# Kernel tuning notes

Measured on AMD Instinct MI355X. Metric: run time of the kernel, lower is better.

## Reference

```python
import jax, jax.numpy as jnp
import numpy as np

B, N, H = 8, 512, 256
D2 = H // 2          # per-direction hidden = attention proj = 128
VOCAB, EMB = 100, 256
DIN0 = EMB + 3


def _sru_pp_layer(x, pad, Wq, Wk, Wv, Wu, vf, vr, bf, br):
    # x: (L, Bt, din); pad: (L, Bt) bool, True = padded position
    L, Bt, _ = x.shape
    d2 = Wu.shape[1] // 8
    q = x @ Wq                                   # (L,Bt,proj) attention projection
    k = q @ Wk
    v = q @ Wv
    scale = 1.0 / jnp.sqrt(jnp.asarray(q.shape[-1], q.dtype))
    scores = jnp.einsum('lbp,mbp->blm', q, k) * scale
    scores = jnp.where(pad.T[:, None, :], -1e9, scores)
    a = jnp.einsum('blm,mbp->lbp', jax.nn.softmax(scores, axis=-1), v) + q
    U = (a @ Wu).reshape(L, Bt, 2, 4, d2)        # 2 directions x 4 matrices

    def run_dir(Ud, padd, vf_d, vr_d, bf_d, br_d):
        def step(c, inp):
            u, p = inp                            # u: (Bt,4,d2), p: (Bt,)
            f = jax.nn.sigmoid(u[:, 1] + vf_d * c + bf_d)
            r = jax.nn.sigmoid(u[:, 2] + vr_d * c + br_d)
            c_new = f * c + (1.0 - f) * u[:, 0]
            c_new = jnp.where(p[:, None], c, c_new)
            h = jnp.where(p[:, None], 0.0, r * c_new + (1.0 - r) * u[:, 3])
            return c_new, h
        c0 = jnp.zeros((Bt, d2), x.dtype)
        _, hs = jax.lax.scan(step, c0, (Ud, padd))
        return hs

    hf = run_dir(U[:, :, 0], pad, vf[0], vr[0], bf[0], br[0])
    hb = run_dir(U[::-1, :, 1], pad[::-1], vf[1], vr[1], bf[1], br[1])[::-1]
    return jnp.concatenate([hf, hb], axis=-1)     # (L,Bt,2*d2)


def _forward(noisy_seqs, noisy_cords, mask, emb, params):
    Bb, Nn = noisy_seqs.shape
    X = noisy_cords[:, :, 1]                      # CA coordinates (B,N,3)
    m3 = mask[..., None]
    center = (X * m3).sum(1) / m3.sum(1)
    Xc = X - center[:, None] * m3
    C = jnp.einsum('bni,bnj->bij', Xc, Xc)        # (B,3,3) covariance
    _, V = jnp.linalg.eigh(jax.lax.stop_gradient(C))
    ops = jnp.asarray([[i, j, k] for i in (-1, 1) for j in (-1, 1) for k in (-1, 1)], X.dtype)
    F_ops = ops[None, :, None, :] * V[:, None]    # (B,8,3,3) sign-flipped frames
    hX = jnp.einsum('boji,bpj->bopi', F_ops, Xc).reshape(Bb * 8, Nn, 3)
    seq = jnp.where(noisy_seqs < 0, 82, noisy_seqs)
    hS = jnp.broadcast_to(emb[seq][:, None], (Bb, 8, Nn, emb.shape[1])).reshape(Bb * 8, Nn, -1)
    h = jnp.swapaxes(jnp.concatenate([hX, hS], -1), 0, 1)   # (N, B*8, EMB+3)
    pad = jnp.broadcast_to((mask == 0.0)[:, None], (Bb, 8, Nn)).reshape(Bb * 8, Nn).T
    for p in params:
        h = _sru_pp_layer(h, pad, *p)
    return jnp.swapaxes(h, 0, 1).reshape(Bb, 8, Nn, -1).mean(1)


def setup_inputs():
    key = jax.random.key(0)
    ks = [jax.random.fold_in(key, i) for i in range(32)]
    inp = {
        'noisy_seqs': jax.random.randint(ks[0], (B, N), 0, VOCAB, dtype=jnp.int32),
        'noisy_cords': jax.random.normal(ks[1], (B, N, 4, 3), jnp.float32),
        'mask': jnp.ones((B, N), jnp.float32),
        'emb': 0.02 * jax.random.normal(ks[2], (VOCAB, EMB), jnp.float32),
    }
    i = 3
    for l, din in enumerate([DIN0, H]):
        inp[f'Wq{l}'] = jax.random.normal(ks[i], (din, D2), jnp.float32) / np.sqrt(din); i += 1
        inp[f'Wk{l}'] = jax.random.normal(ks[i], (D2, D2), jnp.float32) / np.sqrt(D2); i += 1
        inp[f'Wv{l}'] = jax.random.normal(ks[i], (D2, D2), jnp.float32) / np.sqrt(D2); i += 1
        inp[f'Wu{l}'] = jax.random.normal(ks[i], (D2, 8 * D2), jnp.float32) / np.sqrt(D2); i += 1
        inp[f'vf{l}'] = 0.1 * jax.random.normal(ks[i], (2, D2), jnp.float32); i += 1
        inp[f'vr{l}'] = 0.1 * jax.random.normal(ks[i], (2, D2), jnp.float32); i += 1
        inp[f'bf{l}'] = jnp.zeros((2, D2), jnp.float32)
        inp[f'br{l}'] = jnp.zeros((2, D2), jnp.float32)
    return inp


def reference(noisy_seqs, noisy_cords, mask, emb,
              Wq0, Wk0, Wv0, Wu0, vf0, vr0, bf0, br0,
              Wq1, Wk1, Wv1, Wu1, vf1, vr1, bf1, br1):
    params = [(Wq0, Wk0, Wv0, Wu0, vf0, vr0, bf0, br0),
              (Wq1, Wk1, Wv1, Wu1, vf1, vr1, bf1, br1)]
    return _forward(noisy_seqs, noisy_cords, mask, emb, params)
```

## Files before the change

### kernel.cpp

```cpp
#include <hip/hip_runtime.h>
#include <hip/hip_bf16.h>
#include <math.h>

#define L_    512
#define F_    64
#define M_    (F_*L_)
#define D2_   128
#define H_    256
#define LOG2E_ 1.4426950408889634f

typedef unsigned short u16;
typedef __attribute__((ext_vector_type(8))) short s16x8;
typedef __attribute__((ext_vector_type(4))) float f32x4;

__device__ inline u16 bf_hi(float x) {
  union { float f; unsigned u; } v; v.f = x;
  unsigned r = v.u + 0x7fffu + ((v.u >> 16) & 1u);
  return (u16)(r >> 16);
}
__device__ inline float bf_to_f(u16 h) {
  union { float f; unsigned u; } v; v.u = ((unsigned)h) << 16; return v.f;
}
__device__ inline void split2(float x, u16& h, u16& l) {
  h = bf_hi(x);
  l = bf_hi(x - bf_to_f(h));
}
__device__ inline float exp2_fast(float x) {
#if __has_builtin(__builtin_amdgcn_exp2f)
  return __builtin_amdgcn_exp2f(x);
#else
  return __expf(x * 0.6931471805599453f);
#endif
}
__device__ inline float rcp_fast(float x) {
#if __has_builtin(__builtin_amdgcn_rcpf)
  return __builtin_amdgcn_rcpf(x);
#else
  return 1.f/x;
#endif
}

#define RSPLIT_A 18432
#define RSPLIT_B 26624

__global__ void geom_kernel(const float* __restrict__ cords, const float* __restrict__ mask,
                            float* __restrict__ misc) {
  int b = blockIdx.x;
  int t = threadIdx.x;
  __shared__ float red[4][256];
  float sx=0.f, sy=0.f, sz=0.f, sm=0.f;
  for (int l = t; l < 512; l += 256) {
    float m = mask[b*512 + l];
    const float* X = cords + ((size_t)(b*512 + l)*4 + 1)*3;
    sx += X[0]*m; sy += X[1]*m; sz += X[2]*m; sm += m;
  }
  red[0][t]=sx; red[1][t]=sy; red[2][t]=sz; red[3][t]=sm;
  __syncthreads();
  for (int off=128; off>0; off>>=1) {
    if (t < off) { red[0][t]+=red[0][t+off]; red[1][t]+=red[1][t+off];
                   red[2][t]+=red[2][t+off]; red[3][t]+=red[3][t+off]; }
    __syncthreads();
  }
  float inv = 1.f/red[3][0];
  float cx = red[0][0]*inv, cy = red[1][0]*inv, cz = red[2][0]*inv;
  __syncthreads();
  __shared__ float red6[6][256];
  float c00=0,c01=0,c02=0,c11=0,c12=0,c22=0;
  for (int l = t; l < 512; l += 256) {
    float m = mask[b*512+l];
    const float* X = cords + ((size_t)(b*512+l)*4 + 1)*3;
    float x = X[0]-cx*m, y = X[1]-cy*m, z = X[2]-cz*m;
    c00+=x*x; c01+=x*y; c02+=x*z; c11+=y*y; c12+=y*z; c22+=z*z;
  }
  red6[0][t]=c00; red6[1][t]=c01; red6[2][t]=c02;
  red6[3][t]=c11; red6[4][t]=c12; red6[5][t]=c22;
  __syncthreads();
  for (int off=128; off>0; off>>=1) {
    if (t < off) for (int j=0;j<6;j++) red6[j][t]+=red6[j][t+off];
    __syncthreads();
  }
  if (t == 0) {
    double A[3][3], V[3][3];
    A[0][0]=red6[0][0]; A[0][1]=A[1][0]=red6[1][0]; A[0][2]=A[2][0]=red6[2][0];
    A[1][1]=red6[3][0]; A[1][2]=A[2][1]=red6[4][0]; A[2][2]=red6[5][0];
    for (int j=0;j<3;j++) for (int i=0;i<3;i++) V[j][i] = (i==j)?1.0:0.0;
    for (int sweep=0; sweep<10; ++sweep) {
      for (int p=0;p<2;p++) for (int q=p+1;q<3;q++) {
        double apq = A[p][q];
        if (fabs(apq) < 1e-18) continue;
        double app = A[p][p], aqq = A[q][q];
        double tau = (aqq - app) / (2.0*apq);
        double tt = (tau >= 0.0) ? 1.0/(tau + sqrt(1.0+tau*tau))
                                 : 1.0/(tau - sqrt(1.0+tau*tau));
        double cc = 1.0/sqrt(1.0+tt*tt), ss = tt*cc;
        A[p][p] = app - tt*apq;
        A[q][q] = aqq + tt*apq;
        A[p][q] = A[q][p] = 0.0;
        int r = 3 - p - q;
        double arp = A[r][p], arq = A[r][q];
        A[r][p] = A[p][r] = cc*arp - ss*arq;
        A[r][q] = A[q][r] = ss*arp + cc*arq;
        for (int rr2=0; rr2<3; ++rr2) {
          double vrp = V[rr2][p], vrq = V[rr2][q];
          V[rr2][p] = cc*vrp - ss*vrq;
          V[rr2][q] = ss*vrp + cc*vrq;
        }
      }
    }
    double w[3] = {A[0][0], A[1][1], A[2][2]};
    int idx[3] = {0,1,2};
    for (int i=0;i<2;i++) for (int j=0;j<2-i;j++)
      if (w[idx[j]] > w[idx[j+1]]) { int tmp=idx[j]; idx[j]=idx[j+1]; idx[j+1]=tmp; }
    for (int jj=0;jj<3;jj++) for (int ii=0;ii<3;ii++)
      misc[b*12 + jj*3 + ii] = (float)V[jj][idx[ii]];
    misc[b*12+9]=cx; misc[b*12+10]=cy; misc[b*12+11]=cz;
  }
}

__global__ void build_h0(const int* __restrict__ seqs, const float* __restrict__ cords,
                         const float* __restrict__ mask, const float* __restrict__ emb,
                         const float* __restrict__ misc,
                         u16* __restrict__ h0h, u16* __restrict__ h0l) {
  int t = threadIdx.x;
  int r = blockIdx.x*4 + (t >> 6);
  int lane = t & 63;
  int f = r >> 9, l = r & 511;
  int b = f >> 3, o = f & 7;
  u16* rh = h0h + (size_t)r * 288;
  u16* rl = h0l + (size_t)r * 288;
  if (lane == 0) {
    float m = mask[b*512 + l];
    const float* X = cords + ((size_t)(b*512 + l)*4 + 1)*3;
    const float* mb = misc + b*12;
    float x = X[0]-mb[9]*m, y = X[1]-mb[10]*m, z = X[2]-mb[11]*m;
    #pragma unroll
    for (int i=0;i<3;i++) {
      float sgn = ((o >> (2-i)) & 1) ? 1.f : -1.f;
      float val = sgn * (mb[0+i]*x + mb[3+i]*y + mb[6+i]*z);
      u16 h,lo; split2(val,h,lo); rh[i]=h; rl[i]=lo;
    }
  }
  if (lane < 29) { rh[259+lane] = 0; rl[259+lane] = 0; }
  int s = seqs[b*512 + l];
  if (s < 0) s = 82;
  const float4 e4 = *((const float4*)(emb + (size_t)s*256) + lane);
  float ev[4] = {e4.x, e4.y, e4.z, e4.w};
  #pragma unroll
  for (int i=0;i<4;i++) {
    u16 h,lo; split2(ev[i],h,lo);
    rh[3 + lane*4 + i] = h; rl[3 + lane*4 + i] = lo;
  }
}

__global__ void prep_wqkv_mul(const float* __restrict__ Wq, const float* __restrict__ Wk,
                              const float* __restrict__ Wv,
                              float* __restrict__ wqk, float* __restrict__ wqv) {
  int k = blockIdx.x;
  int y = blockIdx.y;
  int t = threadIdx.x;
  __shared__ float row[128];
  row[t] = Wq[(size_t)k*128 + t];
  __syncthreads();
  const float* W2 = y ? Wv : Wk;
  float acc = 0.f;
  for (int j = 0; j < 128; j++) acc += row[j] * W2[(size_t)j*128 + t];
  (y ? wqv : wqk)[(size_t)k*128 + t] = acc;
}

__global__ void prep_wT3(const float* __restrict__ Wq, const float* __restrict__ wqk,
                         const float* __restrict__ wqv,
                         u16* __restrict__ Th, u16* __restrict__ Tl,
                         int K, int KP) {
  int y = blockIdx.y;
  int n = blockIdx.x;
  const float* W = (y==0) ? Wq : (y==1) ? wqk : wqv;
  int row = y*128 + n;
  for (int k = threadIdx.x; k < KP; k += 128) {
    float x = (k < K) ? W[(size_t)k*128 + n] : 0.f;
    u16 h,l; split2(x,h,l);
    Th[(size_t)row*KP + k] = h; Tl[(size_t)row*KP + k] = l;
  }
}

__global__ void prep_wu(const float* __restrict__ Wu, u16* __restrict__ Th, u16* __restrict__ Tl,
                        const float* __restrict__ bfv, const float* __restrict__ brv,
                        float* __restrict__ nbf, float* __restrict__ nbr) {
  int n = blockIdx.x;
  int dir = blockIdx.y;
  int k = threadIdx.x;
  int d = n >> 2, g = n & 3;
  float x = Wu[(size_t)k*1024 + (dir*4+g)*128 + d];
  if (g == 1 || g == 2) x *= -LOG2E_;
  u16 h,l; split2(x,h,l);
  size_t o = ((size_t)dir*512 + n)*128 + k;
  Th[o]=h; Tl[o]=l;
  if (n == 0) {
    nbf[dir*128 + k] = bfv[dir*128 + k] * (-LOG2E_);
    nbr[dir*128 + k] = brv[dir*128 + k] * (-LOG2E_);
  }
}

template<int EPI>
__global__ __launch_bounds__(256) void gemm_bb(
    const u16* __restrict__ Ah, const u16* __restrict__ Al,
    const u16* __restrict__ Bh, const u16* __restrict__ Bl,
    int KP, int lda, int ldb,
    long aBatch, long bBatch, long cBatch,
    u16* __restrict__ Ch, u16* __restrict__ Cl, int ldc,
    u16* __restrict__ Dh, u16* __restrict__ Dl,
    u16* __restrict__ Eh, u16* __restrict__ El,
    float* __restrict__ F0, float* __restrict__ F1, float* __restrict__ F2,
    float* __restrict__ F3, float* __restrict__ F4, float* __restrict__ F5,
    const u16* __restrict__ rh, const u16* __restrict__ rl,
    const float* __restrict__ maskp, const float* __restrict__ nbf,
    const float* __restrict__ nbr, float scale, int dirOff)
{
  __shared__ u16 As[2][128][40];
  __shared__ u16 Bs[2][128][40];
  __shared__ float epsM[128];
  __shared__ float epsA[128];
  const int t = threadIdx.x;
  const int z = blockIdx.z;
  const int bm = blockIdx.x * 128, bn = blockIdx.y * 128;
  Ah += (size_t)z * aBatch; Al += (size_t)z * aBatch;
  Bh += (size_t)z * bBatch; Bl += (size_t)z * bBatch;

  const int lane = t & 63;
  const int w = t >> 6, wr = w >> 1, wc = w & 1;
  const int fr = lane & 15, g = lane >> 4;

  const bool isD1 = (bn >= 512);
  const int dirU = dirOff + (isD1 ? 1 : 0);
  if (EPI == 4) {
    if (t < 128) {
      int r = bm + t;
      epsM[t] = maskp[(r >> 12)*512 + (r & 511)];
      int nl = (bn + t) & 511;
      int dd = nl >> 2, gg2 = nl & 3;
      epsA[t] = (gg2==1) ? nbf[dirU*128 + dd] : (gg2==2) ? nbr[dirU*128 + dd] : 0.f;
    }
  }

  f32x4 acc[4][4] = {};

  for (int k0 = 0; k0 < KP; k0 += 32) {
    #pragma unroll
    for (int cc = 0; cc < 2; cc++) {
      int c = t + cc*256;
      int m = c >> 2, sub = c & 3;
      const size_t ga = (size_t)(bm + m)*lda + k0 + sub*8;
      const size_t gb = (size_t)(bn + m)*ldb + k0 + sub*8;
      *(int4*)&As[0][m][sub*8] = *(const int4*)(Ah + ga);
      *(int4*)&As[1][m][sub*8] = *(const int4*)(Al + ga);
      *(int4*)&Bs[0][m][sub*8] = *(const int4*)(Bh + gb);
      *(int4*)&Bs[1][m][sub*8] = *(const int4*)(Bl + gb);
    }
    __syncthreads();
    s16x8 af[4][2], bfr[4][2];
    #pragma unroll
    for (int i = 0; i < 4; i++) {
      af[i][0]  = *(const s16x8*)&As[0][wr*64 + i*16 + fr][g*8];
      af[i][1]  = *(const s16x8*)&As[1][wr*64 + i*16 + fr][g*8];
      bfr[i][0] = *(const s16x8*)&Bs[0][wc*64 + i*16 + fr][g*8];
      bfr[i][1] = *(const s16x8*)&Bs[1][wc*64 + i*16 + fr][g*8];
    }
    #pragma unroll
    for (int mi = 0; mi < 4; mi++)
      #pragma unroll
      for (int nj = 0; nj < 4; nj++)
        acc[mi][nj] = __builtin_amdgcn_mfma_f32_16x16x32_bf16(af[mi][0], bfr[nj][0], acc[mi][nj], 0,0,0);
    #pragma unroll
    for (int mi = 0; mi < 4; mi++)
      #pragma unroll
      for (int nj = 0; nj < 4; nj++)
        acc[mi][nj] = __builtin_amdgcn_mfma_f32_16x16x32_bf16(af[mi][0], bfr[nj][1], acc[mi][nj], 0,0,0);
    #pragma unroll
    for (int mi = 0; mi < 4; mi++)
      #pragma unroll
      for (int nj = 0; nj < 4; nj++)
        acc[mi][nj] = __builtin_amdgcn_mfma_f32_16x16x32_bf16(af[mi][1], bfr[nj][0], acc[mi][nj], 0,0,0);
    __syncthreads();
  }

  const int rbase = bm + wr*64, nbase = bn + wc*64;
  float* tA = isD1 ? F3 : F0;
  float* tB = isD1 ? F4 : F1;
  float* tC = isD1 ? F5 : F2;
  const int gg = fr & 3;
  const float ovr = (gg==1) ? -16384.f : (gg==2) ? 16384.f : 0.f;

  #pragma unroll
  for (int mi = 0; mi < 4; mi++) {
    #pragma unroll
    for (int nj = 0; nj < 4; nj++) {
      #pragma unroll
      for (int rg = 0; rg < 4; rg++) {
        int r = rbase + mi*16 + g*4 + rg;
        int n = nbase + nj*16 + fr;
        float val = acc[mi][nj][rg];
        if (EPI == 2) {
          float vv = val * scale;
          if (maskp[(z>>3)*512 + n] == 0.f) vv = -1e9f;
          F0[(size_t)z*cBatch + (size_t)r*ldc + n] = vv;
        } else if (EPI == 3) {
          size_t o = (size_t)z*cBatch + (size_t)r*ldc + n;
          float vv = val + (bf_to_f(rh[o]) + bf_to_f(rl[o]));
          u16 h,l; split2(vv,h,l);
          Ch[o]=h; Cl[o]=l;
        } else if (EPI == 4) {
          int nloc = (n & 511);
          val += epsA[n - bn];
          if (epsM[r - bm] == 0.f) val = ovr;
          float* Up;
          if (r < RSPLIT_A)      Up = tA + (size_t)r*512;
          else if (r < RSPLIT_B) Up = tB + (size_t)(r - RSPLIT_A)*512;
          else                   Up = tC + (size_t)(r - RSPLIT_B)*512;
          Up[nloc] = val;
        } else {
          u16 h,l; split2(val,h,l);
          if (blockIdx.y == 0) {
            size_t o = (size_t)r*128 + n;
            Ch[o]=h; Cl[o]=l;
          } else if (blockIdx.y == 1) {
            size_t o = (size_t)r*128 + (n - 128);
            Dh[o]=h; Dl[o]=l;
          } else {
            size_t o = ((size_t)(r >> 9)*128 + (n - 256))*512 + (r & 511);
            Eh[o]=h; El[o]=l;
          }
        }
      }
    }
  }
}

__global__ __launch_bounds__(256) void attn_flash(
    const u16* __restrict__ qh, const u16* __restrict__ ql,
    const u16* __restrict__ kh, const u16* __restrict__ kl,
    const u16* __restrict__ vTh, const u16* __restrict__ vTl,
    const float* __restrict__ maskp,
    u16* __restrict__ ah, u16* __restrict__ al, float scale)
{
  __shared__ u16 As[2][64][36];
  __shared__ u16 Bs[2][128][36];
  __shared__ u16 Ps[2][64][68];
  __shared__ float rmaxL[2][64];
  __shared__ float rsumL[2][64];
  __shared__ float mskt[64];
  const int t = threadIdx.x;
  const int bid = blockIdx.x;
  const int xcd  = bid & 7;
  const int rest = bid >> 3;
  const int tile = rest & 7;
  const int f    = (rest >> 3)*8 + xcd;
  const int bq = f >> 3;
  const int bm = tile * 64;
  const size_t qrow0 = (size_t)f*512 + bm;
  const int lane = t & 63;
  const int w = t >> 6, wr = w >> 1, wc = w & 1;
  const int fr = lane & 15, g = lane >> 4;
  const int m_ = t >> 2, sub_ = t & 3;

  float mrun[2][4], srun[2][4];
  #pragma unroll
  for (int mi=0;mi<2;mi++)
    #pragma unroll
    for (int rg=0;rg<4;rg++) { mrun[mi][rg] = -3e38f; srun[mi][rg] = 0.f; }
  f32x4 Oacc[2][4] = {};

  for (int kt = 0; kt < 8; ++kt) {
    if (t < 64) mskt[t] = maskp[bq*512 + kt*64 + t];
    f32x4 Sacc[2][2] = {};
    #pragma unroll
    for (int k0 = 0; k0 < 4; ++k0) {
      {
        const size_t ga = (qrow0 + m_)*128 + k0*32 + sub_*8;
        const size_t gb = ((size_t)f*512 + kt*64 + m_)*128 + k0*32 + sub_*8;
        *(int4*)&As[0][m_][sub_*8] = *(const int4*)(qh + ga);
        *(int4*)&As[1][m_][sub_*8] = *(const int4*)(ql + ga);
        *(int4*)&Bs[0][m_][sub_*8] = *(const int4*)(kh + gb);
        *(int4*)&Bs[1][m_][sub_*8] = *(const int4*)(kl + gb);
      }
      __syncthreads();
      s16x8 af[2][2], bf2[2][2];
      #pragma unroll
      for (int i = 0; i < 2; i++) {
        af[i][0]  = *(const s16x8*)&As[0][wr*32 + i*16 + fr][g*8];
        af[i][1]  = *(const s16x8*)&As[1][wr*32 + i*16 + fr][g*8];
        bf2[i][0] = *(const s16x8*)&Bs[0][wc*32 + i*16 + fr][g*8];
        bf2[i][1] = *(const s16x8*)&Bs[1][wc*32 + i*16 + fr][g*8];
      }
      #pragma unroll
      for (int mi = 0; mi < 2; mi++)
        #pragma unroll
        for (int nj = 0; nj < 2; nj++)
          Sacc[mi][nj] = __builtin_amdgcn_mfma_f32_16x16x32_bf16(af[mi][0], bf2[nj][0], Sacc[mi][nj], 0,0,0);
      #pragma unroll
      for (int mi = 0; mi < 2; mi++)
        #pragma unroll
        for (int nj = 0; nj < 2; nj++)
          Sacc[mi][nj] = __builtin_amdgcn_mfma_f32_16x16x32_bf16(af[mi][0], bf2[nj][1], Sacc[mi][nj], 0,0,0);
      #pragma unroll
      for (int mi = 0; mi < 2; mi++)
        #pragma unroll
        for (int nj = 0; nj < 2; nj++)
          Sacc[mi][nj] = __builtin_amdgcn_mfma_f32_16x16x32_bf16(af[mi][1], bf2[nj][0], Sacc[mi][nj], 0,0,0);
      __syncthreads();
    }
    float mkv[2];
    mkv[0] = mskt[wc*32 + fr];
    mkv[1] = mskt[wc*32 + 16 + fr];
    float rm[2][4];
    #pragma unroll
    for (int mi=0;mi<2;mi++)
      #pragma unroll
      for (int rg=0;rg<4;rg++) rm[mi][rg] = -3e38f;
    #pragma unroll
    for (int mi=0;mi<2;mi++)
      #pragma unroll
      for (int nj=0;nj<2;nj++)
        #pragma unroll
        for (int rg=0;rg<4;rg++) {
          float sv = Sacc[mi][nj][rg]*scale;
          sv = (mkv[nj]==0.f) ? -1e9f : sv;
          Sacc[mi][nj][rg] = sv;
          rm[mi][rg] = fmaxf(rm[mi][rg], sv);
        }
    #pragma unroll
    for (int off=1; off<16; off<<=1)
      #pragma unroll
      for (int mi=0;mi<2;mi++)
        #pragma unroll
        for (int rg=0;rg<4;rg++) rm[mi][rg] = fmaxf(rm[mi][rg], __shfl_xor(rm[mi][rg], off));
    if (fr == 0) {
      #pragma unroll
      for (int mi=0;mi<2;mi++)
        #pragma unroll
        for (int rg=0;rg<4;rg++) rmaxL[wc][wr*32 + mi*16 + g*4 + rg] = rm[mi][rg];
    }
    __syncthreads();
    float alpha[2][4], rs[2][4];
    #pragma unroll
    for (int mi=0;mi<2;mi++)
      #pragma unroll
      for (int rg=0;rg<4;rg++) {
        int rl_ = wr*32 + mi*16 + g*4 + rg;
        float tmax = fmaxf(rmaxL[0][rl_], rmaxL[1][rl_]);
        float mn = fmaxf(mrun[mi][rg], tmax);
        alpha[mi][rg] = exp2_fast((mrun[mi][rg] - mn)*LOG2E_);
        mrun[mi][rg] = mn;
        rs[mi][rg] = 0.f;
      }
    #pragma unroll
    for (int mi=0;mi<2;mi++)
      #pragma unroll
      for (int nj=0;nj<2;nj++)
        #pragma unroll
        for (int rg=0;rg<4;rg++) {
          float p = exp2_fast((Sacc[mi][nj][rg] - mrun[mi][rg])*LOG2E_);
          rs[mi][rg] += p;
          u16 h,l; split2(p,h,l);
          int rl_ = wr*32 + mi*16 + g*4 + rg;
          int cl_ = wc*32 + nj*16 + fr;
          Ps[0][rl_][cl_] = h;
          Ps[1][rl_][cl_] = l;
        }
    #pragma unroll
    for (int off=1; off<16; off<<=1)
      #pragma unroll
      for (int mi=0;mi<2;mi++)
        #pragma unroll
        for (int rg=0;rg<4;rg++) rs[mi][rg] += __shfl_xor(rs[mi][rg], off);
    if (fr == 0) {
      #pragma unroll
      for (int mi=0;mi<2;mi++)
        #pragma unroll
        for (int rg=0;rg<4;rg++) rsumL[wc][wr*32 + mi*16 + g*4 + rg] = rs[mi][rg];
    }
    #pragma unroll
    for (int mi=0;mi<2;mi++)
      #pragma unroll
      for (int nj=0;nj<4;nj++)
        #pragma unroll
        for (int rg=0;rg<4;rg++) Oacc[mi][nj][rg] *= alpha[mi][rg];
    __syncthreads();
    #pragma unroll
    for (int mi=0;mi<2;mi++)
      #pragma unroll
      for (int rg=0;rg<4;rg++) {
        int rl_ = wr*32 + mi*16 + g*4 + rg;
        srun[mi][rg] = srun[mi][rg]*alpha[mi][rg] + rsumL[0][rl_] + rsumL[1][rl_];
      }
    #pragma unroll
    for (int k0 = 0; k0 < 2; ++k0) {
      #pragma unroll
      for (int cc = 0; cc < 2; cc++) {
        int c = t + cc*256;
        int mv = c >> 2, sb = c & 3;
        const size_t gv = ((size_t)f*128 + mv)*512 + kt*64 + k0*32 + sb*8;
        *(int4*)&Bs[0][mv][sb*8] = *(const int4*)(vTh + gv);
        *(int4*)&Bs[1][mv][sb*8] = *(const int4*)(vTl + gv);
      }
      __syncthreads();
      s16x8 pa[2][2], pb[4][2];
      #pragma unroll
      for (int i = 0; i < 2; i++) {
        pa[i][0] = *(const s16x8*)&Ps[0][wr*32 + i*16 + fr][k0*32 + g*8];
        pa[i][1] = *(const s16x8*)&Ps[1][wr*32 + i*16 + fr][k0*32 + g*8];
      }
      #pragma unroll
      for (int j = 0; j < 4; j++) {
        pb[j][0] = *(const s16x8*)&Bs[0][wc*64 + j*16 + fr][g*8];
        pb[j][1] = *(const s16x8*)&Bs[1][wc*64 + j*16 + fr][g*8];
      }
      #pragma unroll
      for (int mi = 0; mi < 2; mi++)
        #pragma unroll
        for (int nj = 0; nj < 4; nj++)
          Oacc[mi][nj] = __builtin_amdgcn_mfma_f32_16x16x32_bf16(pa[mi][0], pb[nj][0], Oacc[mi][nj], 0,0,0);
      #pragma unroll
      for (int mi = 0; mi < 2; mi++)
        #pragma unroll
        for (int nj = 0; nj < 4; nj++)
          Oacc[mi][nj] = __builtin_amdgcn_mfma_f32_16x16x32_bf16(pa[mi][0], pb[nj][1], Oacc[mi][nj], 0,0,0);
      #pragma unroll
      for (int mi = 0; mi < 2; mi++)
        #pragma unroll
        for (int nj = 0; nj < 4; nj++)
          Oacc[mi][nj] = __builtin_amdgcn_mfma_f32_16x16x32_bf16(pa[mi][1], pb[nj][0], Oacc[mi][nj], 0,0,0);
      __syncthreads();
    }
  }
  float inv[2][4];
  #pragma unroll
  for (int mi=0;mi<2;mi++)
    #pragma unroll
    for (int rg=0;rg<4;rg++) inv[mi][rg] = 1.f / srun[mi][rg];
  #pragma unroll
  for (int mi=0;mi<2;mi++)
    #pragma unroll
    for (int nj=0;nj<4;nj++)
      #pragma unroll
      for (int rg=0;rg<4;rg++) {
        int rl_ = wr*32 + mi*16 + g*4 + rg;
        int cl_ = wc*64 + nj*16 + fr;
        size_t o = (qrow0 + rl_)*128 + cl_;
        float val = Oacc[mi][nj][rg]*inv[mi][rg] + bf_to_f(qh[o]) + bf_to_f(ql[o]);
        u16 h,l; split2(val,h,l);
        ah[o]=h; al[o]=l;
      }
}

__global__ void softmax_split(float* __restrict__ S) {
  size_t row = blockIdx.x;
  float* p = S + row*512;
  u16* ph = (u16*)p;
  u16* pl = ph + 512;
  int t = threadIdx.x;
  float v[8];
  float mx = -1e30f;
  #pragma unroll
  for (int i=0;i<8;i++) { v[i] = p[t + i*64]; mx = fmaxf(mx, v[i]); }
  #pragma unroll
  for (int off=32; off>0; off>>=1) mx = fmaxf(mx, __shfl_xor(mx, off));
  float sum = 0.f;
  #pragma unroll
  for (int i=0;i<8;i++) { v[i] = __expf(v[i]-mx); sum += v[i]; }
  #pragma unroll
  for (int off=32; off>0; off>>=1) sum += __shfl_xor(sum, off);
  float invs = 1.f/sum;
  #pragma unroll
  for (int i=0;i<8;i++) {
    float x = v[i]*invs;
    u16 h,l; split2(x,h,l);
    ph[t + i*64] = h; pl[t + i*64] = l;
  }
}

#define CH_ 8
#define LOADC(buf, ch) do { \
  int _c = (ch); \
  _Pragma("unroll") \
  for (int s = 0; s < CH_; s++) { \
    int l = (_c*CH_ + s) ^ lxor; \
    buf[s] = *(const float4*)(Ubase + (size_t)l*512); \
  } \
  __builtin_amdgcn_sched_barrier(0); \
} while(0)

#define COMPC(buf, ch) do { \
  int _c = (ch); \
  _Pragma("unroll") \
  for (int s = 0; s < CH_; s++) { \
    int l = (_c*CH_ + s) ^ lxor; \
    float4 u = buf[s]; \
    float ef = exp2_fast(fmaf(nvfd, cstate, u.y)); \
    float fg = rcp_fast(1.f + ef); \
    float er = exp2_fast(fmaf(nvrd, cstate, u.z)); \
    float rg = rcp_fast(1.f + er); \
    float cn = fmaf(fg, cstate - u.x, u.x); \
    float h  = fmaf(rg, cn - u.w, u.w); \
    cstate = cn; \
    if (PAIRS) { \
      u16 sh_, sl_; split2(h, sh_, sl_); \
      hpph[(size_t)l*256] = sh_; \
      hppl[(size_t)l*256] = sl_; \
    } else { \
      h32p[(size_t)l*256] = h; \
    } \
  } \
  __builtin_amdgcn_sched_barrier(0); \
} while(0)

template<int PAIRS>
__global__ __launch_bounds__(64, 1) void sru_scan(
                          const float* __restrict__ ua0, const float* __restrict__ ub0,
                          const float* __restrict__ uc0,
                          const float* __restrict__ ua1, const float* __restrict__ ub1,
                          const float* __restrict__ uc1,
                          const float* __restrict__ vf, const float* __restrict__ vr,
                          u16* __restrict__ hph, u16* __restrict__ hpl,
                          float* __restrict__ h32, int dirArg) {
  const int blk = blockIdx.x;
  const int f = blk >> 1;
  const int hh = blk & 1;
  const int dir = dirArg + blockIdx.y;
  const int t = threadIdx.x;
  const int lxor = dir ? 511 : 0;
  const int d = hh*64 + t;
  const float nvfd = vf[dir*128 + d] * (-LOG2E_);
  const float nvrd = vr[dir*128 + d] * (-LOG2E_);
  const size_t fbase = (size_t)f * 512;
  const float* ua = dir ? ua1 : ua0;
  const float* ub = dir ? ub1 : ub0;
  const float* uc = dir ? uc1 : uc0;
  const float* Uf;
  if (f < 36)      Uf = ua + (size_t)f*(512*512);
  else if (f < 52) Uf = ub + (size_t)(f-36)*(512*512);
  else             Uf = uc + (size_t)(f-52)*(512*512);
  const float* Ubase = Uf + d*4;
  u16* hpph = hph + fbase*256 + (size_t)dir*128 + d;
  u16* hppl = hpl + fbase*256 + (size_t)dir*128 + d;
  float* h32p = h32 + fbase*256 + (size_t)dir*128 + d;

  float4 b0[CH_], b1[CH_], b2[CH_], b3[CH_];
  LOADC(b0, 0); LOADC(b1, 1);
  float cstate = 0.f;
  #pragma unroll 1
  for (int q4 = 0; q4 < 15; q4++) {
    const int base = q4*4;
    LOADC(b2, base+2);
    COMPC(b0, base);
    LOADC(b3, base+3);
    COMPC(b1, base+1);
    LOADC(b0, base+4);
    COMPC(b2, base+2);
    LOADC(b1, base+5);
    COMPC(b3, base+3);
  }
  LOADC(b2, 62);
  COMPC(b0, 60);
  LOADC(b3, 63);
  COMPC(b1, 61);
  COMPC(b2, 62);
  COMPC(b3, 63);
}

__global__ void mean_kernel(const float* __restrict__ h2, float* __restrict__ out) {
  int i = blockIdx.x*256 + threadIdx.x;
  int row = i >> 6;
  int c4  = i & 63;
  int b = row >> 9, l = row & 511;
  float ax=0.f, ay=0.f, az=0.f, aw=0.f;
  #pragma unroll
  for (int o=0;o<8;o++) {
    const float4* p = (const float4*)(h2 + ((size_t)((b*8+o)*512 + l))*256) + c4;
    float4 e = *p;
    ax += e.x; ay += e.y; az += e.z; aw += e.w;
  }
  float4 r; r.x = ax*0.125f; r.y = ay*0.125f; r.z = az*0.125f; r.w = aw*0.125f;
  ((float4*)out)[i] = r;
}

extern "C" void kernel_launch(void* const* d_in, const int* in_sizes, int n_in,
                              void* d_out, int out_size, void* d_ws, size_t ws_size,
                              hipStream_t stream) {
  const int*   seqs  = (const int*)d_in[0];
  const float* cords = (const float*)d_in[1];
  const float* mask  = (const float*)d_in[2];
  const float* emb   = (const float*)d_in[3];
  const float* Wq[2] = {(const float*)d_in[4],  (const float*)d_in[12]};
  const float* Wk[2] = {(const float*)d_in[5],  (const float*)d_in[13]};
  const float* Wv[2] = {(const float*)d_in[6],  (const float*)d_in[14]};
  const float* Wu[2] = {(const float*)d_in[7],  (const float*)d_in[15]};
  const float* vf[2] = {(const float*)d_in[8],  (const float*)d_in[16]};
  const float* vr[2] = {(const float*)d_in[9],  (const float*)d_in[17]};
  const float* bfp[2]= {(const float*)d_in[10], (const float*)d_in[18]};
  const float* brp[2]= {(const float*)d_in[11], (const float*)d_in[19]};

  const size_t H0_B = 2*(size_t)M_*288*2;
  const size_t Q_B  = 2*(size_t)M_*128*2;
  const size_t S_B  = (size_t)M_*512*4;
  const size_t HP_B = 2*(size_t)M_*256*2;
  const size_t W_B  = (size_t)(2*1024*128)*2 + 2*256*4;

  const size_t NEED_MERGED = 4096 + H0_B + 3*Q_B + S_B + HP_B + W_B;
  const bool merged = (ws_size >= NEED_MERGED);

  char* base = (char*)d_ws;
  float* misc = (float*)base;
  u16* h0p_h = (u16*)(base + 4096);
  u16* h0p_l = h0p_h + (size_t)M_*288;
  u16* q_h   = (u16*)(base + 4096 + H0_B);
  u16* q_l   = q_h + (size_t)M_*128;
  u16* k_h   = (u16*)(base + 4096 + H0_B + Q_B);
  u16* k_l   = k_h + (size_t)M_*128;

  u16 *vT_h, *vT_l, *a_h, *a_l;
  float *S, *tail_w;
  u16 *hp_h, *hp_l;
  float *U1A, *U1B, *U1C;
  if (merged) {
    vT_h = (u16*)(base + 4096 + H0_B + 2*Q_B);
    vT_l = vT_h + (size_t)M_*128;
    S    = (float*)(base + 4096 + H0_B + 3*Q_B);
    hp_h = (u16*)((char*)S + S_B);
    hp_l = hp_h + (size_t)M_*256;
    tail_w = (float*)((char*)hp_h + HP_B);
    U1A = (float*)h0p_h;
    U1B = (float*)q_h;
    U1C = (float*)vT_h;
    a_h = hp_h;
    a_l = hp_h + (size_t)M_*128;
  } else {
    S    = (float*)(base + 4096 + H0_B + 2*Q_B);
    hp_h = (u16*)((char*)S + S_B);
    hp_l = hp_h + (size_t)M_*256;
    vT_h = hp_h; vT_l = hp_l;
    tail_w = (float*)((char*)hp_h + HP_B);
    U1A = S; U1B = S + (size_t)RSPLIT_A*512; U1C = S + (size_t)RSPLIT_B*512;
    a_h = k_h; a_l = k_l;
  }
  float* U0A = S;
  float* U0B = S + (size_t)RSPLIT_A*512;
  float* U0C = S + (size_t)RSPLIT_B*512;
  float* h32 = (float*)hp_h;

  float* wqk32 = S;
  float* wqv32 = wqk32 + 288*128;
  u16*   wT3h  = (u16*)(wqv32 + 288*128);
  u16*   wT3l  = wT3h + 384*288;
  u16* wuT_h = (u16*)tail_w;
  u16* wuT_l = wuT_h + 1024*128;
  float* nbf = (float*)(wuT_l + 1024*128);
  float* nbr = nbf + 256;

  geom_kernel<<<8, 256, 0, stream>>>(cords, mask, misc);
  build_h0<<<M_/4, 256, 0, stream>>>(seqs, cords, mask, emb, misc, h0p_h, h0p_l);

  const float scale = 0.08838834764831845f;
  for (int layer = 0; layer < 2; ++layer) {
    const u16* Ah_in = layer ? hp_h : h0p_h;
    const u16* Al_in = layer ? hp_l : h0p_l;
    const int  Kq    = layer ? 256 : 259;
    const int  KPq   = layer ? 256 : 288;

    prep_wqkv_mul<<<dim3(Kq,2), 128, 0, stream>>>(Wq[layer], Wk[layer], Wv[layer], wqk32, wqv32);
    prep_wT3<<<dim3(128,3), 128, 0, stream>>>(Wq[layer], wqk32, wqv32, wT3h, wT3l, Kq, KPq);
    prep_wu<<<dim3(512,2), 128, 0, stream>>>(Wu[layer], wuT_h, wuT_l, bfp[layer], brp[layer], nbf, nbr);

    gemm_bb<5><<<dim3(256,3,1), 256, 0, stream>>>(Ah_in, Al_in, wT3h, wT3l,
        KPq, KPq, KPq, 0,0,0, q_h, q_l, 128, k_h, k_l, vT_h, vT_l,
        nullptr,nullptr,nullptr,nullptr,nullptr,nullptr,
        nullptr,nullptr, nullptr,nullptr,nullptr, 0.f, 0);

    if (merged) {
      attn_flash<<<512, 256, 0, stream>>>(q_h, q_l, k_h, k_l, vT_h, vT_l,
          mask, a_h, a_l, scale);
    } else {
      gemm_bb<2><<<dim3(4,4,64), 256, 0, stream>>>(q_h, q_l, k_h, k_l,
          128, 128, 128, 512*128, 512*128, 512*512, nullptr,nullptr, 512,
          nullptr,nullptr,nullptr,nullptr,
          S,nullptr,nullptr,nullptr,nullptr,nullptr,
          nullptr,nullptr, mask,nullptr,nullptr, scale, 0);
      softmax_split<<<M_, 64, 0, stream>>>(S);
      gemm_bb<3><<<dim3(4,1,64), 256, 0, stream>>>((const u16*)S, (const u16*)S + 512, vT_h, vT_l,
          512, 1024, 512, 512*1024, 128*512, 512*128, a_h, a_l, 128,
          nullptr,nullptr,nullptr,nullptr,
          nullptr,nullptr,nullptr,nullptr,nullptr,nullptr,
          q_h, q_l, nullptr,nullptr,nullptr, 0.f, 0);
    }

    if (merged) {
      gemm_bb<4><<<dim3(256,8,1), 256, 0, stream>>>(a_h, a_l, wuT_h, wuT_l,
          128, 128, 128, 0,0,0, nullptr,nullptr, 512,
          nullptr,nullptr,nullptr,nullptr,
          U0A,U0B,U0C, U1A,U1B,U1C,
          nullptr,nullptr, mask, nbf, nbr, 0.f, 0);
      if (layer == 0)
        sru_scan<1><<<dim3(128,2), 64, 0, stream>>>(U0A,U0B,U0C, U1A,U1B,U1C,
            vf[layer], vr[layer], hp_h, hp_l, h32, 0);
      else
        sru_scan<0><<<dim3(128,2), 64, 0, stream>>>(U0A,U0B,U0C, U1A,U1B,U1C,
            vf[layer], vr[layer], hp_h, hp_l, h32, 0);
    } else {
      for (int dir = 0; dir < 2; ++dir) {
        gemm_bb<4><<<dim3(256,4,1), 256, 0, stream>>>(a_h, a_l,
            wuT_h + (size_t)dir*512*128, wuT_l + (size_t)dir*512*128,
            128, 128, 128, 0,0,0, nullptr,nullptr, 512,
            nullptr,nullptr,nullptr,nullptr,
            U0A,U0B,U0C, U0A,U0B,U0C,
            nullptr,nullptr, mask, nbf, nbr, 0.f, dir);
        if (layer == 0)
          sru_scan<1><<<dim3(128,1), 64, 0, stream>>>(U0A,U0B,U0C, U0A,U0B,U0C,
              vf[layer], vr[layer], hp_h, hp_l, h32, dir);
        else
          sru_scan<0><<<dim3(128,1), 64, 0, stream>>>(U0A,U0B,U0C, U0A,U0B,U0C,
              vf[layer], vr[layer], hp_h, hp_l, h32, dir);
      }
    }
  }
  mean_kernel<<<1024, 256, 0, stream>>>(h32, (float*)d_out);
}
```

Before: 449.7 us.

## Keep Q fragments in registers and stage full K/V tiles once per block

Measured after the change: 470.2 us. 1.05x slower.

```diff
diff --git a/kernel.cpp b/kernel.cpp
--- a/kernel.cpp
+++ b/kernel.cpp
@@ -341,8 +341,7 @@
     const float* __restrict__ maskp,
     u16* __restrict__ ah, u16* __restrict__ al, float scale)
 {
-  __shared__ u16 As[2][64][36];
-  __shared__ u16 Bs[2][128][36];
+  __shared__ __align__(16) u16 KV[2*8704];
   __shared__ u16 Ps[2][64][68];
   __shared__ float rmaxL[2][64];
   __shared__ float rsumL[2][64];
@@ -359,7 +358,17 @@
   const int lane = t & 63;
   const int w = t >> 6, wr = w >> 1, wc = w & 1;
   const int fr = lane & 15, g = lane >> 4;
-  const int m_ = t >> 2, sub_ = t & 3;
+
+  s16x8 qf[2][4][2];
+  #pragma unroll
+  for (int i = 0; i < 2; i++) {
+    const size_t qr = (qrow0 + wr*32 + i*16 + fr)*128;
+    #pragma unroll
+    for (int k0 = 0; k0 < 4; k0++) {
+      qf[i][k0][0] = *(const s16x8*)(qh + qr + k0*32 + g*8);
+      qf[i][k0][1] = *(const s16x8*)(ql + qr + k0*32 + g*8);
+    }
+  }
 
   float mrun[2][4], srun[2][4];
   #pragma unroll
@@ -370,43 +379,45 @@
 
   for (int kt = 0; kt < 8; ++kt) {
     if (t < 64) mskt[t] = maskp[bq*512 + kt*64 + t];
+    #pragma unroll
+    for (int p = 0; p < 2; p++) {
+      const u16* src = p ? kl : kh;
+      #pragma unroll
+      for (int ii = 0; ii < 4; ii++) {
+        int id = ii*256 + t;
+        int row = id >> 4, c = (id & 15)*8;
+        *(int4*)&KV[p*8448 + row*132 + c] =
+          *(const int4*)(src + ((size_t)f*512 + kt*64 + row)*128 + c);
+      }
+    }
+    __syncthreads();
     f32x4 Sacc[2][2] = {};
+    __builtin_amdgcn_s_setprio(1);
     #pragma unroll
     for (int k0 = 0; k0 < 4; ++k0) {
-      {
-        const size_t ga = (qrow0 + m_)*128 + k0*32 + sub_*8;
-        const size_t gb = ((size_t)f*512 + kt*64 + m_)*128 + k0*32 + sub_*8;
-        *(int4*)&As[0][m_][sub_*8] = *(const int4*)(qh + ga);
-        *(int4*)&As[1][m_][sub_*8] = *(const int4*)(ql + ga);
-        *(int4*)&Bs[0][m_][sub_*8] = *(const int4*)(kh + gb);
-        *(int4*)&Bs[1][m_][sub_*8] = *(const int4*)(kl + gb);
-      }
-      __syncthreads();
-      s16x8 af[2][2], bf2[2][2];
-      #pragma unroll
-      for (int i = 0; i < 2; i++) {
-        af[i][0]  = *(const s16x8*)&As[0][wr*32 + i*16 + fr][g*8];
-        af[i][1]  = *(const s16x8*)&As[1][wr*32 + i*16 + fr][g*8];
-        bf2[i][0] = *(const s16x8*)&Bs[0][wc*32 + i*16 + fr][g*8];
-        bf2[i][1] = *(const s16x8*)&Bs[1][wc*32 + i*16 + fr][g*8];
+      s16x8 bf2[2][2];
+      #pragma unroll
+      for (int nj = 0; nj < 2; nj++) {
+        bf2[nj][0] = *(const s16x8*)&KV[        (wc*32 + nj*16 + fr)*132 + k0*32 + g*8];
+        bf2[nj][1] = *(const s16x8*)&KV[8448 + (wc*32 + nj*16 + fr)*132 + k0*32 + g*8];
       }
       #pragma unroll
       for (int mi = 0; mi < 2; mi++)
         #pragma unroll
         for (int nj = 0; nj < 2; nj++)
-          Sacc[mi][nj] = __builtin_amdgcn_mfma_f32_16x16x32_bf16(af[mi][0], bf2[nj][0], Sacc[mi][nj], 0,0,0);
+          Sacc[mi][nj] = __builtin_amdgcn_mfma_f32_16x16x32_bf16(qf[mi][k0][0], bf2[nj][0], Sacc[mi][nj], 0,0,0);
       #pragma unroll
       for (int mi = 0; mi < 2; mi++)
         #pragma unroll
         for (int nj = 0; nj < 2; nj++)
-          Sacc[mi][nj] = __builtin_amdgcn_mfma_f32_16x16x32_bf16(af[mi][0], bf2[nj][1], Sacc[mi][nj], 0,0,0);
+          Sacc[mi][nj] = __builtin_amdgcn_mfma_f32_16x16x32_bf16(qf[mi][k0][0], bf2[nj][1], Sacc[mi][nj], 0,0,0);
       #pragma unroll
       for (int mi = 0; mi < 2; mi++)
         #pragma unroll
         for (int nj = 0; nj < 2; nj++)
-          Sacc[mi][nj] = __builtin_amdgcn_mfma_f32_16x16x32_bf16(af[mi][1], bf2[nj][0], Sacc[mi][nj], 0,0,0);
-      __syncthreads();
-    }
+          Sacc[mi][nj] = __builtin_amdgcn_mfma_f32_16x16x32_bf16(qf[mi][k0][1], bf2[nj][0], Sacc[mi][nj], 0,0,0);
+    }
+    __builtin_amdgcn_s_setprio(0);
     float mkv[2];
     mkv[0] = mskt[wc*32 + fr];
     mkv[1] = mskt[wc*32 + 16 + fr];
@@ -492,16 +503,20 @@
         srun[mi][rg] = srun[mi][rg]*alpha[mi][rg] + rsumL[0][rl_] + rsumL[1][rl_];
       }
     #pragma unroll
+    for (int p = 0; p < 2; p++) {
+      const u16* src = p ? vTl : vTh;
+      #pragma unroll
+      for (int ii = 0; ii < 4; ii++) {
+        int id = ii*256 + t;
+        int d = id >> 3, c = (id & 7)*8;
+        *(int4*)&KV[p*8704 + d*68 + c] =
+          *(const int4*)(src + ((size_t)f*128 + d)*512 + kt*64 + c);
+      }
+    }
+    __syncthreads();
+    __builtin_amdgcn_s_setprio(1);
+    #pragma unroll
     for (int k0 = 0; k0 < 2; ++k0) {
-      #pragma unroll
-      for (int cc = 0; cc < 2; cc++) {
-        int c = t + cc*256;
-        int mv = c >> 2, sb = c & 3;
-        const size_t gv = ((size_t)f*128 + mv)*512 + kt*64 + k0*32 + sb*8;
-        *(int4*)&Bs[0][mv][sb*8] = *(const int4*)(vTh + gv);
-        *(int4*)&Bs[1][mv][sb*8] = *(const int4*)(vTl + gv);
-      }
-      __syncthreads();
       s16x8 pa[2][2], pb[4][2];
       #pragma unroll
       for (int i = 0; i < 2; i++) {
@@ -510,8 +525,8 @@
       }
       #pragma unroll
       for (int j = 0; j < 4; j++) {
-        pb[j][0] = *(const s16x8*)&Bs[0][wc*64 + j*16 + fr][g*8];
-        pb[j][1] = *(const s16x8*)&Bs[1][wc*64 + j*16 + fr][g*8];
+        pb[j][0] = *(const s16x8*)&KV[        (wc*64 + j*16 + fr)*68 + k0*32 + g*8];
+        pb[j][1] = *(const s16x8*)&KV[8704 + (wc*64 + j*16 + fr)*68 + k0*32 + g*8];
       }
       #pragma unroll
       for (int mi = 0; mi < 2; mi++)
@@ -528,8 +543,9 @@
         #pragma unroll
         for (int nj = 0; nj < 4; nj++)
           Oacc[mi][nj] = __builtin_amdgcn_mfma_f32_16x16x32_bf16(pa[mi][1], pb[nj][0], Oacc[mi][nj], 0,0,0);
-      __syncthreads();
-    }
+    }
+    __builtin_amdgcn_s_setprio(0);
+    __syncthreads();
   }
   float inv[2][4];
   #pragma unroll
```
